# Performance work log

Measured on AMD Instinct MI355X. Metric: run time of the kernel, lower is better.

The kernel has to match this reference:

```python
import jax, jax.numpy as jnp
import numpy as np

N, E, B = 100_000, 1_000_000, 16
H = 16  # hidden width from layers=(16,16,1)


def setup_inputs() -> dict:
    key = jax.random.key(0)
    ks = iter(jax.random.split(key, 40))
    def randn(shape):
        return jax.random.normal(next(ks), shape, dtype=jnp.float32)
    def w(shape):
        fan_in = shape[0]
        return randn(shape) / np.sqrt(fan_in)
    inp = {
        'x': randn((N, 1)),
        'e': randn((E, 1)),
        'g': randn((B, 1)),
        # encoder: independent MLPs on raw 1-dim features
        'We_enc': w((1, H)), 'be_enc': jnp.zeros((H,), jnp.float32),
        'Wx_enc': w((1, H)), 'bx_enc': jnp.zeros((H,), jnp.float32),
        'Wg_enc': w((1, 1)), 'bg_enc': jnp.zeros((1,), jnp.float32),
        # core: edge in = 32(e)+32(src)+32(dst)+2(g)=98; node in = 32+16+2=50; global in = 2+16+16=34
        'We_core': w((98, H)), 'be_core': jnp.zeros((H,), jnp.float32),
        'Wx_core': w((50, H)), 'bx_core': jnp.zeros((H,), jnp.float32),
        'Wg_core': w((34, 1)), 'bg_core': jnp.zeros((1,), jnp.float32),
        # decoder: independent MLPs
        'We_dec': w((H, H)), 'be_dec': jnp.zeros((H,), jnp.float32),
        'Wx_dec': w((H, H)), 'bx_dec': jnp.zeros((H,), jnp.float32),
        'Wg_dec': w((1, 1)), 'bg_dec': jnp.zeros((1,), jnp.float32),
        # output transform: plain Linear
        'We_out': w((H, 2)), 'be_out': jnp.zeros((2,), jnp.float32),
        'Wx_out': w((H, 2)), 'bx_out': jnp.zeros((2,), jnp.float32),
        'Wg_out': w((1, 1)), 'bg_out': jnp.zeros((1,), jnp.float32),
        'edges': jax.random.randint(next(ks), (2, E), 0, N),
        'node_idx': jnp.sort(jax.random.randint(next(ks), (N,), 0, B)),
        'edge_idx': jnp.sort(jax.random.randint(next(ks), (E,), 0, B)),
        'steps': 2,
    }
    return inp


def reference(x, e, g,
              We_enc, be_enc, Wx_enc, bx_enc, Wg_enc, bg_enc,
              We_core, be_core, Wx_core, bx_core, Wg_core, bg_core,
              We_dec, be_dec, Wx_dec, bx_dec, Wg_dec, bg_dec,
              We_out, be_out, Wx_out, bx_out, Wg_out, bg_out,
              edges, node_idx, edge_idx, steps):
    relu = jax.nn.relu
    src, dst = edges[0], edges[1]

    # ---- encoder (independent blocks) ----
    e1 = relu(e @ We_enc + be_enc)   # [E,16]
    x1 = relu(x @ Wx_enc + bx_enc)   # [N,16]
    g1 = relu(g @ Wg_enc + bg_enc)   # [B,1]
    ec, xc, gc = e1, x1, g1

    # per-dst edge counts for scatter-mean
    counts = jax.ops.segment_sum(jnp.ones((e.shape[0], 1), jnp.float32), dst, num_segments=N)
    counts = jnp.maximum(counts, 1.0)

    outs_e, outs_x, outs_g = [], [], []
    for _ in range(steps):
        # concat latent0 with current latent
        e_in = jnp.concatenate([e1, ec], axis=1)  # [E,32]
        x_in = jnp.concatenate([x1, xc], axis=1)  # [N,32]
        g_in = jnp.concatenate([g1, gc], axis=1)  # [B,2]

        # ---- core ----
        # edge block: gather src/dst nodes and per-edge globals
        e_feat = jnp.concatenate([e_in, x_in[src], x_in[dst], g_in[edge_idx]], axis=1)  # [E,98]
        e_new = relu(e_feat @ We_core + be_core)  # [E,16]
        # node block: mean-aggregate new edges onto destination nodes
        agg_e = jax.ops.segment_sum(e_new, dst, num_segments=N) / counts  # [N,16]
        x_feat = jnp.concatenate([x_in, agg_e, g_in[node_idx]], axis=1)   # [N,50]
        x_new = relu(x_feat @ Wx_core + bx_core)  # [N,16]
        # global block: add-aggregate nodes and edges per graph
        node_agg = jax.ops.segment_sum(x_new, node_idx, num_segments=B)   # [B,16]
        edge_agg = jax.ops.segment_sum(e_new, edge_idx, num_segments=B)   # [B,16]
        g_feat = jnp.concatenate([g_in, node_agg, edge_agg], axis=1)      # [B,34]
        g_new = relu(g_feat @ Wg_core + bg_core)  # [B,1]
        ec, xc, gc = e_new, x_new, g_new

        # ---- decoder (independent) ----
        ed = relu(ec @ We_dec + be_dec)
        xd = relu(xc @ Wx_dec + bx_dec)
        gd = relu(gc @ Wg_dec + bg_dec)

        # ---- output transform (plain linear) ----
        outs_e.append(ed @ We_out + be_out)  # [E,2]
        outs_x.append(xd @ Wx_out + bx_out)  # [N,2]
        outs_g.append(gd @ Wg_out + bg_out)  # [B,1]

    return (jnp.stack(outs_e), jnp.stack(outs_x), jnp.stack(outs_g))
```

## Files before the change

### kernel.cpp

```cpp
#include <hip/hip_runtime.h>

#define DEV __device__ __forceinline__

DEV float relu(float v) { return v > 0.f ? v : 0.f; }

#define G1_OFF 0
#define GIN_OFF 16
#define WEE 48
#define BEE 64
#define WC  80
#define BC  1648
#define WD  1664
#define BD  1920
#define WO  1936
#define BO  1968
#define WXE 1972
#define BXE 1988
#define WXC 2004
#define BXC 2804
#define WXD 2820
#define BXD 3076
#define WXO 3092
#define BXO 3124
#define WGE 3126
#define BGE 3127
#define WGC 3128
#define BGC 3162
#define WGD 3163
#define BGD 3164
#define WGO 3165
#define BGO 3166
#define SMALL_N 3200

struct P {
    const float *x, *e, *g;
    const int *src, *dst, *nidx, *eidx;
    float *ec, *xin, *small, *eagg_rep, *nagg_rep;
    int *cnt, *rowptr, *cursor, *colidx;
    float *out;
    int N, E, B;
};

struct WIn {
    const float *we_enc, *be_enc, *wx_enc, *bx_enc, *wg_enc, *bg_enc;
    const float *wc, *bc, *wxc, *bxc, *wgc, *bgc;
    const float *wd, *bd, *wxd, *bxd, *wgd, *bgd;
    const float *wo, *bo, *wxo, *bxo, *wgo, *bgo;
};

__global__ __launch_bounds__(256) void k_init_small(P p, WIn w) {
    int t = threadIdx.x;
    float* S = p.small;
#define CP(ptr, off, len) for (int i = t; i < (len); i += 256) S[(off) + i] = ptr[i];
    CP(w.we_enc, WEE, 16) CP(w.be_enc, BEE, 16)
    CP(w.wc, WC, 1568)    CP(w.bc, BC, 16)
    CP(w.wd, WD, 256)     CP(w.bd, BD, 16)
    CP(w.wo, WO, 32)      CP(w.bo, BO, 2)
    CP(w.wx_enc, WXE, 16) CP(w.bx_enc, BXE, 16)
    CP(w.wxc, WXC, 800)   CP(w.bxc, BXC, 16)
    CP(w.wxd, WXD, 256)   CP(w.bxd, BXD, 16)
    CP(w.wxo, WXO, 32)    CP(w.bxo, BXO, 2)
    CP(w.wgc, WGC, 34)
#undef CP
    if (t == 0) {
        S[WGE] = w.wg_enc[0]; S[BGE] = w.bg_enc[0];
        S[BGC] = w.bgc[0];
        S[WGD] = w.wgd[0];    S[BGD] = w.bgd[0];
        S[WGO] = w.wgo[0];    S[BGO] = w.bgo[0];
    }
    if (t < p.B) {
        float gv = p.g[t];
        float g1 = relu(gv * w.wg_enc[0] + w.bg_enc[0]);
        S[G1_OFF + t] = g1;
        S[GIN_OFF + 2 * t] = g1;
        S[GIN_OFF + 2 * t + 1] = g1;
    }
    for (int r = t; r < 16 * 256; r += 256) p.nagg_rep[r] = 0.f;
    for (int r = t; r < 64 * 256; r += 256) p.eagg_rep[r] = 0.f;
}

__global__ __launch_bounds__(256) void k_init_nodes(P p, WIn w) {
    size_t n = (size_t)blockIdx.x * 256 + threadIdx.x;
    if (n >= (size_t)p.N) return;
    p.cnt[n] = 0;
    float xv = p.x[n];
    float* row = p.xin + n * 32;
#pragma unroll
    for (int h = 0; h < 16; h++) {
        float v = relu(xv * w.wx_enc[h] + w.bx_enc[h]);
        row[h] = v;
        row[16 + h] = v;
    }
}

__global__ __launch_bounds__(256) void k_hist(P p) {
    size_t i = (size_t)blockIdx.x * 256 + threadIdx.x;
    if (i >= (size_t)p.E) return;
    atomicAdd(&p.cnt[p.dst[i]], 1);
}

#define SCAN_T 1024
#define SCAN_V 4
__global__ __launch_bounds__(SCAN_T) void k_scan(P p) {
    __shared__ int wsum[16];
    __shared__ int carry_s;
    int t = threadIdx.x;
    int lane = t & 63, wid = t >> 6;
    if (t == 0) carry_s = 0;
    __syncthreads();
    int chunk = SCAN_T * SCAN_V;
    int nchunk = (p.N + chunk - 1) / chunk;
    for (int c = 0; c < nchunk; c++) {
        int base = c * chunk + t * SCAN_V;
        int v[SCAN_V];
        int s = 0;
#pragma unroll
        for (int k = 0; k < SCAN_V; k++) {
            int idx = base + k;
            v[k] = (idx < p.N) ? p.cnt[idx] : 0;
            s += v[k];
        }
        int incl = s;
#pragma unroll
        for (int off = 1; off < 64; off <<= 1) {
            int u = __shfl_up(incl, off);
            if (lane >= off) incl += u;
        }
        if (lane == 63) wsum[wid] = incl;
        __syncthreads();
        if (wid == 0) {
            int ws = (lane < 16) ? wsum[lane] : 0;
            int wincl = ws;
#pragma unroll
            for (int off = 1; off < 16; off <<= 1) {
                int u = __shfl_up(wincl, off);
                if (lane >= off) wincl += u;
            }
            if (lane < 16) wsum[lane] = wincl - ws;
        }
        __syncthreads();
        int carry = carry_s;
        int excl = carry + wsum[wid] + incl - s;
        int run = excl;
#pragma unroll
        for (int k = 0; k < SCAN_V; k++) {
            int idx = base + k;
            if (idx < p.N) { p.rowptr[idx] = run; p.cursor[idx] = run; }
            run += v[k];
        }
        __syncthreads();
        if (t == SCAN_T - 1) carry_s = excl + s;
        __syncthreads();
    }
    if (t == 0) p.rowptr[p.N] = carry_s;
}

__global__ __launch_bounds__(256) void k_scatter(P p) {
    size_t i = (size_t)blockIdx.x * 256 + threadIdx.x;
    if (i >= (size_t)p.E) return;
    int d = p.dst[i];
    int slot = atomicAdd(&p.cursor[d], 1);
    p.colidx[slot] = (int)i;
}

template <int STEP0>
__global__ __launch_bounds__(256) void k_edge(P p, int s) {
    const size_t i = (size_t)blockIdx.x * 256 + threadIdx.x;
    const bool valid = i < (size_t)p.E;
    const float* __restrict__ S = p.small;
    float enew[16];
    int b = 0;
    if (valid) {
        float acc[16];
#pragma unroll
        for (int h = 0; h < 16; h++) acc[h] = S[BC + h];
        float ev = p.e[i];
        float e1v[16];
#pragma unroll
        for (int h = 0; h < 16; h++) e1v[h] = relu(ev * S[WEE + h] + S[BEE + h]);
#pragma unroll
        for (int j = 0; j < 16; j++)
#pragma unroll
            for (int h = 0; h < 16; h++) acc[h] += e1v[j] * S[WC + j * 16 + h];
        if (STEP0) {
#pragma unroll
            for (int j = 0; j < 16; j++)
#pragma unroll
                for (int h = 0; h < 16; h++) acc[h] += e1v[j] * S[WC + (16 + j) * 16 + h];
        } else {
            const float4* ecv = (const float4*)(p.ec + i * 16);
#pragma unroll
            for (int c = 0; c < 4; c++) {
                float4 v = ecv[c];
                float vv[4] = {v.x, v.y, v.z, v.w};
#pragma unroll
                for (int k = 0; k < 4; k++)
#pragma unroll
                    for (int h = 0; h < 16; h++) acc[h] += vv[k] * S[WC + (16 + c * 4 + k) * 16 + h];
            }
        }
        int si = p.src[i], di = p.dst[i];
        const float4* xs = (const float4*)(p.xin + (size_t)si * 32);
#pragma unroll
        for (int c = 0; c < 8; c++) {
            float4 v = xs[c];
            float vv[4] = {v.x, v.y, v.z, v.w};
#pragma unroll
            for (int k = 0; k < 4; k++)
#pragma unroll
                for (int h = 0; h < 16; h++) acc[h] += vv[k] * S[WC + (32 + c * 4 + k) * 16 + h];
        }
        const float4* xd = (const float4*)(p.xin + (size_t)di * 32);
#pragma unroll
        for (int c = 0; c < 8; c++) {
            float4 v = xd[c];
            float vv[4] = {v.x, v.y, v.z, v.w};
#pragma unroll
            for (int k = 0; k < 4; k++)
#pragma unroll
                for (int h = 0; h < 16; h++) acc[h] += vv[k] * S[WC + (64 + c * 4 + k) * 16 + h];
        }
        b = p.eidx[i];
        float g0 = S[GIN_OFF + 2 * b], gcv = S[GIN_OFF + 2 * b + 1];
#pragma unroll
        for (int h = 0; h < 16; h++) acc[h] += g0 * S[WC + 96 * 16 + h] + gcv * S[WC + 97 * 16 + h];
#pragma unroll
        for (int h = 0; h < 16; h++) enew[h] = relu(acc[h]);
        float4* eco = (float4*)(p.ec + i * 16);
#pragma unroll
        for (int c = 0; c < 4; c++)
            eco[c] = make_float4(enew[c * 4], enew[c * 4 + 1], enew[c * 4 + 2], enew[c * 4 + 3]);
        float d[16];
#pragma unroll
        for (int h2 = 0; h2 < 16; h2++) d[h2] = S[BD + h2];
#pragma unroll
        for (int h = 0; h < 16; h++)
#pragma unroll
            for (int h2 = 0; h2 < 16; h2++) d[h2] += enew[h] * S[WD + h * 16 + h2];
        float o0 = S[BO], o1 = S[BO + 1];
#pragma unroll
        for (int h2 = 0; h2 < 16; h2++) {
            float dv = relu(d[h2]);
            o0 += dv * S[WO + h2 * 2];
            o1 += dv * S[WO + h2 * 2 + 1];
        }
        ((float2*)p.out)[(size_t)s * p.E + i] = make_float2(o0, o1);
    } else {
#pragma unroll
        for (int h = 0; h < 16; h++) enew[h] = 0.f;
    }
    int b0 = __shfl(b, 0);
    bool uni = __all(!valid || b == b0);
    float* rep = p.eagg_rep + (size_t)(blockIdx.x & 63) * 256;
    if (uni) {
#pragma unroll
        for (int h = 0; h < 16; h++) {
            float v = enew[h];
            v += __shfl_down(v, 32); v += __shfl_down(v, 16); v += __shfl_down(v, 8);
            v += __shfl_down(v, 4);  v += __shfl_down(v, 2);  v += __shfl_down(v, 1);
            if ((threadIdx.x & 63) == 0) atomicAdd(rep + b0 * 16 + h, v);
        }
    } else if (valid) {
#pragma unroll
        for (int h = 0; h < 16; h++) atomicAdd(rep + b * 16 + h, enew[h]);
    }
}

__global__ __launch_bounds__(256) void k_node(P p, int s) {
    const size_t n = (size_t)blockIdx.x * 256 + threadIdx.x;
    const bool valid = n < (size_t)p.N;
    const float* __restrict__ S = p.small;
    float xnew[16];
    int b = 0;
    if (valid) {
        float acc[16];
#pragma unroll
        for (int h = 0; h < 16; h++) acc[h] = S[BXC + h];
        float xv = p.x[n];
        float x1v[16];
#pragma unroll
        for (int h = 0; h < 16; h++) x1v[h] = relu(xv * S[WXE + h] + S[BXE + h]);
#pragma unroll
        for (int j = 0; j < 16; j++)
#pragma unroll
            for (int h = 0; h < 16; h++) acc[h] += x1v[j] * S[WXC + j * 16 + h];
        const float4* xcv = (const float4*)(p.xin + n * 32 + 16);
#pragma unroll
        for (int c = 0; c < 4; c++) {
            float4 v = xcv[c];
            float vv[4] = {v.x, v.y, v.z, v.w};
#pragma unroll
            for (int k = 0; k < 4; k++)
#pragma unroll
                for (int h = 0; h < 16; h++) acc[h] += vv[k] * S[WXC + (16 + c * 4 + k) * 16 + h];
        }
        int start = p.rowptr[n], end = p.rowptr[n + 1];
        int cnt = end - start;
        float inv = (cnt > 0) ? 1.f / (float)cnt : 1.f;
        float sum[16];
#pragma unroll
        for (int k = 0; k < 16; k++) sum[k] = 0.f;
        for (int j = start; j < end; j++) {
            int eid = p.colidx[j];
            const float4* er = (const float4*)(p.ec + (size_t)eid * 16);
            float4 a = er[0], b4 = er[1], c4 = er[2], d4 = er[3];
            sum[0] += a.x;  sum[1] += a.y;  sum[2] += a.z;  sum[3] += a.w;
            sum[4] += b4.x; sum[5] += b4.y; sum[6] += b4.z; sum[7] += b4.w;
            sum[8] += c4.x; sum[9] += c4.y; sum[10] += c4.z; sum[11] += c4.w;
            sum[12] += d4.x; sum[13] += d4.y; sum[14] += d4.z; sum[15] += d4.w;
        }
#pragma unroll
        for (int k = 0; k < 16; k++) {
            float av = sum[k] * inv;
#pragma unroll
            for (int h = 0; h < 16; h++) acc[h] += av * S[WXC + (32 + k) * 16 + h];
        }
        b = p.nidx[n];
        float g0 = S[GIN_OFF + 2 * b], gcv = S[GIN_OFF + 2 * b + 1];
#pragma unroll
        for (int h = 0; h < 16; h++) acc[h] += g0 * S[WXC + 48 * 16 + h] + gcv * S[WXC + 49 * 16 + h];
#pragma unroll
        for (int h = 0; h < 16; h++) xnew[h] = relu(acc[h]);
        float4* xo = (float4*)(p.xin + n * 32 + 16);
#pragma unroll
        for (int c = 0; c < 4; c++)
            xo[c] = make_float4(xnew[c * 4], xnew[c * 4 + 1], xnew[c * 4 + 2], xnew[c * 4 + 3]);
        float d[16];
#pragma unroll
        for (int h2 = 0; h2 < 16; h2++) d[h2] = S[BXD + h2];
#pragma unroll
        for (int h = 0; h < 16; h++)
#pragma unroll
            for (int h2 = 0; h2 < 16; h2++) d[h2] += xnew[h] * S[WXD + h * 16 + h2];
        float o0 = S[BXO], o1 = S[BXO + 1];
#pragma unroll
        for (int h2 = 0; h2 < 16; h2++) {
            float dv = relu(d[h2]);
            o0 += dv * S[WXO + h2 * 2];
            o1 += dv * S[WXO + h2 * 2 + 1];
        }
        ((float2*)p.out)[(size_t)2 * p.E + (size_t)s * p.N + n] = make_float2(o0, o1);
    } else {
#pragma unroll
        for (int h = 0; h < 16; h++) xnew[h] = 0.f;
    }
    int b0 = __shfl(b, 0);
    bool uni = __all(!valid || b == b0);
    float* rep = p.nagg_rep + (size_t)(blockIdx.x & 15) * 256;
    if (uni) {
#pragma unroll
        for (int h = 0; h < 16; h++) {
            float v = xnew[h];
            v += __shfl_down(v, 32); v += __shfl_down(v, 16); v += __shfl_down(v, 8);
            v += __shfl_down(v, 4);  v += __shfl_down(v, 2);  v += __shfl_down(v, 1);
            if ((threadIdx.x & 63) == 0) atomicAdd(rep + b0 * 16 + h, v);
        }
    } else if (valid) {
#pragma unroll
        for (int h = 0; h < 16; h++) atomicAdd(rep + b * 16 + h, xnew[h]);
    }
}

__global__ __launch_bounds__(256) void k_global(P p, int s) {
    __shared__ float na[256], ea[256];
    int t = threadIdx.x;
    float sn = 0.f, se = 0.f;
    for (int r = 0; r < 16; r++) sn += p.nagg_rep[r * 256 + t];
    for (int r = 0; r < 64; r++) se += p.eagg_rep[r * 256 + t];
    na[t] = sn;
    ea[t] = se;
    __syncthreads();
    if (t < p.B) {
        const float* S = p.small;
        float g0 = S[GIN_OFF + 2 * t], gcv = S[GIN_OFF + 2 * t + 1];
        float acc = S[BGC] + g0 * S[WGC + 0] + gcv * S[WGC + 1];
#pragma unroll
        for (int h = 0; h < 16; h++) acc += na[t * 16 + h] * S[WGC + 2 + h];
#pragma unroll
        for (int h = 0; h < 16; h++) acc += ea[t * 16 + h] * S[WGC + 18 + h];
        float gn = relu(acc);
        p.small[GIN_OFF + 2 * t + 1] = gn;
        float gd = relu(gn * S[WGD] + S[BGD]);
        float og = gd * S[WGO] + S[BGO];
        p.out[(size_t)4 * p.E + (size_t)4 * p.N + (size_t)s * p.B + t] = og;
    }
    __syncthreads();
    for (int r = t; r < 16 * 256; r += 256) p.nagg_rep[r] = 0.f;
    for (int r = t; r < 64 * 256; r += 256) p.eagg_rep[r] = 0.f;
}

extern "C" void kernel_launch(void* const* d_in, const int* in_sizes, int n_in,
                              void* d_out, int out_size, void* d_ws, size_t ws_size,
                              hipStream_t stream) {
    int N = in_sizes[0], E = in_sizes[1], B = in_sizes[2];
    P p;
    p.x = (const float*)d_in[0];
    p.e = (const float*)d_in[1];
    p.g = (const float*)d_in[2];
    const int* edges = (const int*)d_in[27];
    p.src = edges;
    p.dst = edges + E;
    p.nidx = (const int*)d_in[28];
    p.eidx = (const int*)d_in[29];

    float* ws = (float*)d_ws;
    size_t off = 0;
    p.ec = ws + off;        off += (size_t)E * 16;
    p.xin = ws + off;       off += (size_t)N * 32;
    p.eagg_rep = ws + off;  off += 64 * 256;
    p.nagg_rep = ws + off;  off += 16 * 256;
    p.small = ws + off;     off += SMALL_N;
    p.cnt = (int*)(ws + off);    off += N;
    p.rowptr = (int*)(ws + off); off += (size_t)N + 1;
    p.cursor = (int*)(ws + off); off += N;
    p.colidx = (int*)(ws + off); off += E;
    p.out = (float*)d_out;
    p.N = N; p.E = E; p.B = B;

    WIn w;
    w.we_enc = (const float*)d_in[3];  w.be_enc = (const float*)d_in[4];
    w.wx_enc = (const float*)d_in[5];  w.bx_enc = (const float*)d_in[6];
    w.wg_enc = (const float*)d_in[7];  w.bg_enc = (const float*)d_in[8];
    w.wc = (const float*)d_in[9];      w.bc = (const float*)d_in[10];
    w.wxc = (const float*)d_in[11];    w.bxc = (const float*)d_in[12];
    w.wgc = (const float*)d_in[13];    w.bgc = (const float*)d_in[14];
    w.wd = (const float*)d_in[15];     w.bd = (const float*)d_in[16];
    w.wxd = (const float*)d_in[17];    w.bxd = (const float*)d_in[18];
    w.wgd = (const float*)d_in[19];    w.bgd = (const float*)d_in[20];
    w.wo = (const float*)d_in[21];     w.bo = (const float*)d_in[22];
    w.wxo = (const float*)d_in[23];    w.bxo = (const float*)d_in[24];
    w.wgo = (const float*)d_in[25];    w.bgo = (const float*)d_in[26];

    int nb = (N + 255) / 256, eb = (E + 255) / 256;
    k_init_small<<<1, 256, 0, stream>>>(p, w);
    k_init_nodes<<<nb, 256, 0, stream>>>(p, w);
    k_hist<<<eb, 256, 0, stream>>>(p);
    k_scan<<<1, SCAN_T, 0, stream>>>(p);
    k_scatter<<<eb, 256, 0, stream>>>(p);
    for (int s = 0; s < 2; s++) {
        if (s == 0) k_edge<1><<<eb, 256, 0, stream>>>(p, s);
        else        k_edge<0><<<eb, 256, 0, stream>>>(p, s);
        k_node<<<nb, 256, 0, stream>>>(p, s);
        k_global<<<1, 256, 0, stream>>>(p, s);
    }
}
```

Before: 859.3 us.

## Process edges in destination-sorted order and aggregate per-graph sums in LDS

Adds a permute pass that reorders edge features, source/graph indices (packed) and destinations into CSR order, so the edge kernel writes ec in destination-sorted order. The node kernel can then read contiguous edge rows without the colidx indirection. Per-graph edge sums are now accumulated in a shared-memory table before one global atomic per slot. The cost is an extra kernel and three E-sized buffers. Output writes become scattered through colidx, and the edge kernel's loads of the 1-dim edge feature and indices now follow sorted order, which breaks the original edge-order locality.

```diff
diff --git a/kernel.cpp b/kernel.cpp
--- a/kernel.cpp
+++ b/kernel.cpp
@@ -37,6 +37,9 @@
     const int *src, *dst, *nidx, *eidx;
     float *ec, *xin, *small, *eagg_rep, *nagg_rep;
     int *cnt, *rowptr, *cursor, *colidx;
+    float *eperm;
+    int *spk;
+    int *dstperm;
     float *out;
     int N, E, B;
 };
@@ -163,32 +166,46 @@
     p.colidx[slot] = (int)i;
 }
 
+__global__ __launch_bounds__(256) void k_permute(P p) {
+    size_t j = (size_t)blockIdx.x * 256 + threadIdx.x;
+    if (j >= (size_t)p.E) return;
+    int i = p.colidx[j];
+    p.eperm[j] = p.e[i];
+    p.spk[j] = p.src[i] | (p.eidx[i] << 24);
+    p.dstperm[j] = p.dst[i];
+}
+
 template <int STEP0>
 __global__ __launch_bounds__(256) void k_edge(P p, int s) {
-    const size_t i = (size_t)blockIdx.x * 256 + threadIdx.x;
-    const bool valid = i < (size_t)p.E;
+    __shared__ float eagg_lds[16 * 17];
+    const int t = threadIdx.x;
+    for (int r = t; r < 16 * 17; r += 256) eagg_lds[r] = 0.f;
+    __syncthreads();
+    const size_t j = (size_t)blockIdx.x * 256 + t;
     const float* __restrict__ S = p.small;
-    float enew[16];
-    int b = 0;
-    if (valid) {
+    if (j < (size_t)p.E) {
         float acc[16];
 #pragma unroll
         for (int h = 0; h < 16; h++) acc[h] = S[BC + h];
-        float ev = p.e[i];
+        float ev = p.eperm[j];
+        unsigned sp = (unsigned)p.spk[j];
+        int si = (int)(sp & 0xFFFFFFu);
+        int b = (int)(sp >> 24);
+        int di = p.dstperm[j];
         float e1v[16];
 #pragma unroll
         for (int h = 0; h < 16; h++) e1v[h] = relu(ev * S[WEE + h] + S[BEE + h]);
 #pragma unroll
-        for (int j = 0; j < 16; j++)
-#pragma unroll
-            for (int h = 0; h < 16; h++) acc[h] += e1v[j] * S[WC + j * 16 + h];
+        for (int jj = 0; jj < 16; jj++)
+#pragma unroll
+            for (int h = 0; h < 16; h++) acc[h] += e1v[jj] * S[WC + jj * 16 + h];
         if (STEP0) {
 #pragma unroll
-            for (int j = 0; j < 16; j++)
-#pragma unroll
-                for (int h = 0; h < 16; h++) acc[h] += e1v[j] * S[WC + (16 + j) * 16 + h];
+            for (int jj = 0; jj < 16; jj++)
+#pragma unroll
+                for (int h = 0; h < 16; h++) acc[h] += e1v[jj] * S[WC + (16 + jj) * 16 + h];
         } else {
-            const float4* ecv = (const float4*)(p.ec + i * 16);
+            const float4* ecv = (const float4*)(p.ec + j * 16);
 #pragma unroll
             for (int c = 0; c < 4; c++) {
                 float4 v = ecv[c];
@@ -199,7 +216,6 @@
                     for (int h = 0; h < 16; h++) acc[h] += vv[k] * S[WC + (16 + c * 4 + k) * 16 + h];
             }
         }
-        int si = p.src[i], di = p.dst[i];
         const float4* xs = (const float4*)(p.xin + (size_t)si * 32);
 #pragma unroll
         for (int c = 0; c < 8; c++) {
@@ -220,16 +236,19 @@
 #pragma unroll
                 for (int h = 0; h < 16; h++) acc[h] += vv[k] * S[WC + (64 + c * 4 + k) * 16 + h];
         }
-        b = p.eidx[i];
         float g0 = S[GIN_OFF + 2 * b], gcv = S[GIN_OFF + 2 * b + 1];
 #pragma unroll
         for (int h = 0; h < 16; h++) acc[h] += g0 * S[WC + 96 * 16 + h] + gcv * S[WC + 97 * 16 + h];
+        float enew[16];
 #pragma unroll
         for (int h = 0; h < 16; h++) enew[h] = relu(acc[h]);
-        float4* eco = (float4*)(p.ec + i * 16);
+        float4* eco = (float4*)(p.ec + j * 16);
 #pragma unroll
         for (int c = 0; c < 4; c++)
             eco[c] = make_float4(enew[c * 4], enew[c * 4 + 1], enew[c * 4 + 2], enew[c * 4 + 3]);
+#pragma unroll
+        for (int h = 0; h < 16; h++) atomicAdd(&eagg_lds[b * 17 + h], enew[h]);
+        int i = p.colidx[j];
         float d[16];
 #pragma unroll
         for (int h2 = 0; h2 < 16; h2++) d[h2] = S[BD + h2];
@@ -245,24 +264,12 @@
             o1 += dv * S[WO + h2 * 2 + 1];
         }
         ((float2*)p.out)[(size_t)s * p.E + i] = make_float2(o0, o1);
-    } else {
-#pragma unroll
-        for (int h = 0; h < 16; h++) enew[h] = 0.f;
-    }
-    int b0 = __shfl(b, 0);
-    bool uni = __all(!valid || b == b0);
-    float* rep = p.eagg_rep + (size_t)(blockIdx.x & 63) * 256;
-    if (uni) {
-#pragma unroll
-        for (int h = 0; h < 16; h++) {
-            float v = enew[h];
-            v += __shfl_down(v, 32); v += __shfl_down(v, 16); v += __shfl_down(v, 8);
-            v += __shfl_down(v, 4);  v += __shfl_down(v, 2);  v += __shfl_down(v, 1);
-            if ((threadIdx.x & 63) == 0) atomicAdd(rep + b0 * 16 + h, v);
-        }
-    } else if (valid) {
-#pragma unroll
-        for (int h = 0; h < 16; h++) atomicAdd(rep + b * 16 + h, enew[h]);
+    }
+    __syncthreads();
+    {
+        float v = eagg_lds[(t >> 4) * 17 + (t & 15)];
+        if (v != 0.f)
+            atomicAdd(p.eagg_rep + (size_t)(blockIdx.x & 63) * 256 + t, v);
     }
 }
 
@@ -281,9 +288,9 @@
 #pragma unroll
         for (int h = 0; h < 16; h++) x1v[h] = relu(xv * S[WXE + h] + S[BXE + h]);
 #pragma unroll
-        for (int j = 0; j < 16; j++)
-#pragma unroll
-            for (int h = 0; h < 16; h++) acc[h] += x1v[j] * S[WXC + j * 16 + h];
+        for (int jj = 0; jj < 16; jj++)
+#pragma unroll
+            for (int h = 0; h < 16; h++) acc[h] += x1v[jj] * S[WXC + jj * 16 + h];
         const float4* xcv = (const float4*)(p.xin + n * 32 + 16);
 #pragma unroll
         for (int c = 0; c < 4; c++) {
@@ -300,9 +307,8 @@
         float sum[16];
 #pragma unroll
         for (int k = 0; k < 16; k++) sum[k] = 0.f;
-        for (int j = start; j < end; j++) {
-            int eid = p.colidx[j];
-            const float4* er = (const float4*)(p.ec + (size_t)eid * 16);
+        for (int jj = start; jj < end; jj++) {
+            const float4* er = (const float4*)(p.ec + (size_t)jj * 16);
             float4 a = er[0], b4 = er[1], c4 = er[2], d4 = er[3];
             sum[0] += a.x;  sum[1] += a.y;  sum[2] += a.z;  sum[3] += a.w;
             sum[4] += b4.x; sum[5] += b4.y; sum[6] += b4.z; sum[7] += b4.w;
@@ -410,10 +416,13 @@
     p.eagg_rep = ws + off;  off += 64 * 256;
     p.nagg_rep = ws + off;  off += 16 * 256;
     p.small = ws + off;     off += SMALL_N;
-    p.cnt = (int*)(ws + off);    off += N;
-    p.rowptr = (int*)(ws + off); off += (size_t)N + 1;
-    p.cursor = (int*)(ws + off); off += N;
-    p.colidx = (int*)(ws + off); off += E;
+    p.cnt = (int*)(ws + off);     off += N;
+    p.rowptr = (int*)(ws + off);  off += (size_t)N + 1;
+    p.cursor = (int*)(ws + off);  off += N;
+    p.colidx = (int*)(ws + off);  off += E;
+    p.eperm = ws + off;           off += E;
+    p.spk = (int*)(ws + off);     off += E;
+    p.dstperm = (int*)(ws + off); off += E;
     p.out = (float*)d_out;
     p.N = N; p.E = E; p.B = B;
 
@@ -437,6 +446,7 @@
     k_hist<<<eb, 256, 0, stream>>>(p);
     k_scan<<<1, SCAN_T, 0, stream>>>(p);
     k_scatter<<<eb, 256, 0, stream>>>(p);
+    k_permute<<<eb, 256, 0, stream>>>(p);
     for (int s = 0; s < 2; s++) {
         if (s == 0) k_edge<1><<<eb, 256, 0, stream>>>(p, s);
         else        k_edge<0><<<eb, 256, 0, stream>>>(p, s);
```

New measurement: 826.9 us. -3.8%, faster.
